# Optimization experiments

Hardware: AMD Instinct MI355X
Metric: run time of the kernel (lower is better)

## Reference

```python
import jax, jax.numpy as jnp
import numpy as np

RES = (20, 20)
SIGMA = 0.1


def setup_inputs() -> dict:
    key = jax.random.key(0)
    # [batch, num_dims, max_points, 2] birth/death coords in [0,1)
    pd = jax.random.uniform(key, (32, 3, 2048, 2), dtype=jnp.float32)
    return {"persistence_diagrams": pd}


def reference(persistence_diagrams) -> jnp.ndarray:
    # births/deaths: [B, D, P]
    births = persistence_diagrams[..., 0]
    deaths = persistence_diagrams[..., 1]
    pers = deaths - births  # persistence; also the default weight function
    # Original loop skips all-zero rows and points with persistence <= 0.
    # An all-zero row has persistence == 0, so (pers > 0) subsumes both checks.
    eff_w = jnp.where(pers > 0, pers, 0.0)  # [B, D, P]

    x_range = jnp.linspace(0.0, 1.0, RES[0], dtype=jnp.float32)
    y_range = jnp.linspace(0.0, 1.0, RES[1], dtype=jnp.float32)
    xx, yy = jnp.meshgrid(x_range, y_range, indexing="ij")  # [Rx, Ry]

    # Splat each point's Gaussian centered at (birth, persistence) onto the grid.
    # d2: [B, D, P, Rx, Ry]
    d2 = (xx - births[..., None, None]) ** 2 + (yy - pers[..., None, None]) ** 2
    gauss = jnp.exp(-d2 / (2.0 * SIGMA ** 2))
    # Weighted sum over points -> [B, D, Rx, Ry]
    image = jnp.einsum("bdpxy,bdp->bdxy", gauss, eff_w)
    return image
```

## Files before the change

### kernel.cpp

```cpp
#include <hip/hip_runtime.h>


#define RX 20
#define RY 20
#define SPLIT 8
#define CHUNK 256
#define STRIDE 22

__global__ __launch_bounds__(256) void pimg_kernel(const float2* __restrict__ pd,
                                                   float* __restrict__ out,
                                                   int n_bd) {
    __shared__ __attribute__((aligned(16))) float s_gxw[CHUNK * STRIDE];
    __shared__ __attribute__((aligned(16))) float s_gy[CHUNK * STRIDE];
    __shared__ int s_wave_cnt[4];

    const int tid   = threadIdx.x;
    const int bd    = blockIdx.x / SPLIT;
    const int chunk = blockIdx.x % SPLIT;
    const int pbase = bd * 2048 + chunk * CHUNK;

    float2 p2  = pd[pbase + tid];
    float birth = p2.x;
    float pers  = p2.y - p2.x;
    bool active = pers > 0.0f;

    unsigned long long mask = __ballot(active);
    int lane = tid & 63;
    int wid  = tid >> 6;
    int rank = __popcll(mask & ((1ull << lane) - 1ull));
    if (lane == 0) s_wave_cnt[wid] = __popcll(mask);
    __syncthreads();

    int offset = 0;
    #pragma unroll
    for (int w = 0; w < 4; ++w)
        if (w < wid) offset += s_wave_cnt[w];
    int total = s_wave_cnt[0] + s_wave_cnt[1] + s_wave_cnt[2] + s_wave_cnt[3];

    if (active) {
        int slot = offset + rank;
        #pragma unroll
        for (int i = 0; i < RX; ++i) {
            float xi = i * (1.0f / 19.0f);
            float dx = xi - birth;
            float dy = xi - pers;
            s_gxw[slot * STRIDE + i] = pers * __expf(-50.0f * dx * dx);
            s_gy [slot * STRIDE + i] =        __expf(-50.0f * dy * dy);
        }
    }
    __syncthreads();

    if (tid < 200) {
        int i  = tid / 10;
        int j0 = (tid % 10) * 2;
        float acc0 = 0.0f, acc1 = 0.0f;
        #pragma unroll 4
        for (int p = 0; p < total; ++p) {
            float  gx = s_gxw[p * STRIDE + i];
            float2 gy = *(const float2*)&s_gy[p * STRIDE + j0];
            acc0 = fmaf(gx, gy.x, acc0);
            acc1 = fmaf(gx, gy.y, acc1);
        }
        float* o = out + (bd * RX + i) * RY + j0;
        atomicAdd(o,     acc0);
        atomicAdd(o + 1, acc1);
    }
}

extern "C" void kernel_launch(void* const* d_in, const int* in_sizes, int n_in,
                              void* d_out, int out_size, void* d_ws, size_t ws_size,
                              hipStream_t stream) {
    const float2* pd = (const float2*)d_in[0];
    float* out = (float*)d_out;
    int n_bd = in_sizes[0] / (2048 * 2);
    hipMemsetAsync(d_out, 0, (size_t)out_size * sizeof(float), stream);
    pimg_kernel<<<dim3(n_bd * SPLIT), dim3(256), 0, stream>>>(pd, out, n_bd);
}
```

Baseline: 60.44 us.

## Transpose shared tables and use 2x2 register tiles with split-K reduction

Stores the per-point Gaussian factors transposed (grid index major, point index minor) so each thread can read float4 runs of points. Each thread now computes a 2x2 output tile, and two thread halves split the point range and then combine their partial sums through shared memory before the atomics. This aims to cut LDS load instructions per FMA and to use all 256 threads instead of 200. The cost is zero-padding writes to reach a multiple of four points, an extra barrier, and a strided transposed write pattern that may cause bank conflicts.

```diff
diff --git a/kernel.cpp b/kernel.cpp
--- a/kernel.cpp
+++ b/kernel.cpp
@@ -5,14 +5,15 @@
 #define RY 20
 #define SPLIT 8
 #define CHUNK 256
-#define STRIDE 22
+#define PST 260
 
 __global__ __launch_bounds__(256) void pimg_kernel(const float2* __restrict__ pd,
                                                    float* __restrict__ out,
                                                    int n_bd) {
-    __shared__ __attribute__((aligned(16))) float s_gxw[CHUNK * STRIDE];
-    __shared__ __attribute__((aligned(16))) float s_gy[CHUNK * STRIDE];
+    __shared__ __attribute__((aligned(16))) float s_gxT[RX * PST];
+    __shared__ __attribute__((aligned(16))) float s_gyT[RY * PST];
     __shared__ int s_wave_cnt[4];
+    __shared__ float s_red[100 * 5];
 
     const int tid   = threadIdx.x;
     const int bd    = blockIdx.x / SPLIT;
@@ -36,6 +37,7 @@
     for (int w = 0; w < 4; ++w)
         if (w < wid) offset += s_wave_cnt[w];
     int total = s_wave_cnt[0] + s_wave_cnt[1] + s_wave_cnt[2] + s_wave_cnt[3];
+    int tp = (total + 3) & ~3;
 
     if (active) {
         int slot = offset + rank;
@@ -44,26 +46,65 @@
             float xi = i * (1.0f / 19.0f);
             float dx = xi - birth;
             float dy = xi - pers;
-            s_gxw[slot * STRIDE + i] = pers * __expf(-50.0f * dx * dx);
-            s_gy [slot * STRIDE + i] =        __expf(-50.0f * dy * dy);
+            s_gxT[i * PST + slot] = pers * __expf(-50.0f * dx * dx);
+            s_gyT[i * PST + slot] =        __expf(-50.0f * dy * dy);
+        }
+    }
+    if (tid >= total && tid < tp) {
+        #pragma unroll
+        for (int i = 0; i < RX; ++i) {
+            s_gxT[i * PST + tid] = 0.0f;
+            s_gyT[i * PST + tid] = 0.0f;
         }
     }
     __syncthreads();
 
-    if (tid < 200) {
-        int i  = tid / 10;
-        int j0 = (tid % 10) * 2;
-        float acc0 = 0.0f, acc1 = 0.0f;
-        #pragma unroll 4
-        for (int p = 0; p < total; ++p) {
-            float  gx = s_gxw[p * STRIDE + i];
-            float2 gy = *(const float2*)&s_gy[p * STRIDE + j0];
-            acc0 = fmaf(gx, gy.x, acc0);
-            acc1 = fmaf(gx, gy.y, acc1);
+    const int half = tid >> 7;
+    const int t100 = tid & 127;
+    float a00 = 0.0f, a01 = 0.0f, a10 = 0.0f, a11 = 0.0f;
+    int ig = 0, jg = 0;
+    if (t100 < 100) {
+        ig = t100 / 10;
+        jg = t100 % 10;
+        int s_mid = (tp >> 1) & ~3;
+        int s0 = half ? s_mid : 0;
+        int s1 = half ? tp    : s_mid;
+        const float* gxa = &s_gxT[ ig       * PST];
+        const float* gxb = &s_gxT[(ig + 10) * PST];
+        const float* gya = &s_gyT[ jg       * PST];
+        const float* gyb = &s_gyT[(jg + 10) * PST];
+        for (int s = s0; s < s1; s += 4) {
+            float4 xa = *(const float4*)(gxa + s);
+            float4 xb = *(const float4*)(gxb + s);
+            float4 ya = *(const float4*)(gya + s);
+            float4 yb = *(const float4*)(gyb + s);
+            a00 = fmaf(xa.x, ya.x, a00); a00 = fmaf(xa.y, ya.y, a00);
+            a00 = fmaf(xa.z, ya.z, a00); a00 = fmaf(xa.w, ya.w, a00);
+            a01 = fmaf(xa.x, yb.x, a01); a01 = fmaf(xa.y, yb.y, a01);
+            a01 = fmaf(xa.z, yb.z, a01); a01 = fmaf(xa.w, yb.w, a01);
+            a10 = fmaf(xb.x, ya.x, a10); a10 = fmaf(xb.y, ya.y, a10);
+            a10 = fmaf(xb.z, ya.z, a10); a10 = fmaf(xb.w, ya.w, a10);
+            a11 = fmaf(xb.x, yb.x, a11); a11 = fmaf(xb.y, yb.y, a11);
+            a11 = fmaf(xb.z, yb.z, a11); a11 = fmaf(xb.w, yb.w, a11);
         }
-        float* o = out + (bd * RX + i) * RY + j0;
-        atomicAdd(o,     acc0);
-        atomicAdd(o + 1, acc1);
+    }
+    if (half == 1 && t100 < 100) {
+        s_red[t100 * 5 + 0] = a00;
+        s_red[t100 * 5 + 1] = a01;
+        s_red[t100 * 5 + 2] = a10;
+        s_red[t100 * 5 + 3] = a11;
+    }
+    __syncthreads();
+    if (half == 0 && t100 < 100) {
+        a00 += s_red[t100 * 5 + 0];
+        a01 += s_red[t100 * 5 + 1];
+        a10 += s_red[t100 * 5 + 2];
+        a11 += s_red[t100 * 5 + 3];
+        float* o = out + bd * (RX * RY);
+        atomicAdd(o +  ig       * RY + jg,      a00);
+        atomicAdd(o +  ig       * RY + jg + 10, a01);
+        atomicAdd(o + (ig + 10) * RY + jg,      a10);
+        atomicAdd(o + (ig + 10) * RY + jg + 10, a11);
     }
 }
 
```

After: 59.00 us (median of 2 runs). 1.02x faster.

## Transpose Gaussian tables, use register-tiled outer product with wave-split reduction

Applied to the files above, without the earlier changes.

Stores the x and y Gaussian factors transposed (grid index major, point minor) so the accumulation loop can read float4 vectors along points. Each lane computes a 2x4 register tile of outputs, and the point range is split across the four waves, with a shared-memory reduction before the atomics. The exponentials are now produced by a recurrence that multiplies by precomputed ratios, so only four expf calls are made per half-row instead of twenty. The recurrence can drift numerically, and the extra reduction pass adds a barrier and more shared memory.

```diff
diff --git a/kernel.cpp b/kernel.cpp
--- a/kernel.cpp
+++ b/kernel.cpp
@@ -5,65 +5,123 @@
 #define RY 20
 #define SPLIT 8
 #define CHUNK 256
-#define STRIDE 22
+#define PST 260
+#define H (1.0f / 19.0f)
+
+#define FMA4(acc, xv, yv)                                        \
+    acc = fmaf(xv.x, yv.x, acc); acc = fmaf(xv.y, yv.y, acc);    \
+    acc = fmaf(xv.z, yv.z, acc); acc = fmaf(xv.w, yv.w, acc);
 
 __global__ __launch_bounds__(256) void pimg_kernel(const float2* __restrict__ pd,
                                                    float* __restrict__ out,
                                                    int n_bd) {
-    __shared__ __attribute__((aligned(16))) float s_gxw[CHUNK * STRIDE];
-    __shared__ __attribute__((aligned(16))) float s_gy[CHUNK * STRIDE];
-    __shared__ int s_wave_cnt[4];
+    __shared__ __attribute__((aligned(16))) float s_gxT[RX * PST];
+    __shared__ __attribute__((aligned(16))) float s_gyT[RY * PST];
+    __shared__ float2 s_pts[CHUNK];
+    __shared__ float  s_red[3 * 50 * 9];
+    __shared__ int    s_wave_cnt[4];
 
-    const int tid   = threadIdx.x;
+    const int tid  = threadIdx.x;
+    const int lane = tid & 63;
+    const int wid  = tid >> 6;
     const int bd    = blockIdx.x / SPLIT;
     const int chunk = blockIdx.x % SPLIT;
     const int pbase = bd * 2048 + chunk * CHUNK;
 
-    float2 p2  = pd[pbase + tid];
+    float2 p2   = pd[pbase + tid];
     float birth = p2.x;
     float pers  = p2.y - p2.x;
     bool active = pers > 0.0f;
 
     unsigned long long mask = __ballot(active);
-    int lane = tid & 63;
-    int wid  = tid >> 6;
-    int rank = __popcll(mask & ((1ull << lane) - 1ull));
     if (lane == 0) s_wave_cnt[wid] = __popcll(mask);
     __syncthreads();
 
-    int offset = 0;
+    int offset = 0, total = 0;
     #pragma unroll
-    for (int w = 0; w < 4; ++w)
-        if (w < wid) offset += s_wave_cnt[w];
-    int total = s_wave_cnt[0] + s_wave_cnt[1] + s_wave_cnt[2] + s_wave_cnt[3];
+    for (int w = 0; w < 4; ++w) {
+        int c = s_wave_cnt[w];
+        if (w < wid) offset += c;
+        total += c;
+    }
+    int tp = (total + 3) & ~3;
+    if (active) {
+        int rank = __popcll(mask & ((1ull << lane) - 1ull));
+        s_pts[offset + rank] = make_float2(birth, pers);
+    }
+    if (tid >= total && tid < tp)
+        s_pts[tid] = make_float2(0.0f, 0.0f);
+    __syncthreads();
 
-    if (active) {
-        int slot = offset + rank;
-        #pragma unroll
-        for (int i = 0; i < RX; ++i) {
-            float xi = i * (1.0f / 19.0f);
-            float dx = xi - birth;
-            float dy = xi - pers;
-            s_gxw[slot * STRIDE + i] = pers * __expf(-50.0f * dx * dx);
-            s_gy [slot * STRIDE + i] =        __expf(-50.0f * dy * dy);
+    {
+        const int ibase = (tid & 1) * 10;
+        const float rc = __expf(-100.0f * H * H);
+        for (int s = tid >> 1; s < tp; s += 128) {
+            float2 bp = s_pts[s];
+            float b = bp.x, q = bp.y;
+            float dx = ibase * H - b;
+            float dy = ibase * H - q;
+            float fx = __expf(-50.0f * dx * dx);
+            float fy = __expf(-50.0f * dy * dy);
+            float gx = __expf(-100.0f * H * dx - 50.0f * H * H);
+            float gy = __expf(-100.0f * H * dy - 50.0f * H * H);
+            #pragma unroll
+            for (int ii = 0; ii < 10; ++ii) {
+                s_gxT[(ibase + ii) * PST + s] = q * fx;
+                s_gyT[(ibase + ii) * PST + s] = fy;
+                fx *= gx; gx *= rc;
+                fy *= gy; gy *= rc;
+            }
         }
     }
     __syncthreads();
 
-    if (tid < 200) {
-        int i  = tid / 10;
-        int j0 = (tid % 10) * 2;
-        float acc0 = 0.0f, acc1 = 0.0f;
-        #pragma unroll 4
-        for (int p = 0; p < total; ++p) {
-            float  gx = s_gxw[p * STRIDE + i];
-            float2 gy = *(const float2*)&s_gy[p * STRIDE + j0];
-            acc0 = fmaf(gx, gy.x, acc0);
-            acc1 = fmaf(gx, gy.y, acc1);
+    float a[2][4] = {{0.0f, 0.0f, 0.0f, 0.0f}, {0.0f, 0.0f, 0.0f, 0.0f}};
+    const int i0 = lane / 5;
+    const int j0 = lane % 5;
+    if (lane < 50) {
+        int qs = (((tp + 3) >> 2) + 3) & ~3;
+        int s0 = wid * qs; if (s0 > tp) s0 = tp;
+        int s1 = s0 + qs;  if (s1 > tp) s1 = tp;
+        const float* gxa = &s_gxT[ i0        * PST];
+        const float* gxb = &s_gxT[(i0 + 10)  * PST];
+        const float* gy0 = &s_gyT[ j0        * PST];
+        const float* gy1 = &s_gyT[(j0 + 5)   * PST];
+        const float* gy2 = &s_gyT[(j0 + 10)  * PST];
+        const float* gy3 = &s_gyT[(j0 + 15)  * PST];
+        for (int s = s0; s < s1; s += 4) {
+            float4 xa = *(const float4*)(gxa + s);
+            float4 xb = *(const float4*)(gxb + s);
+            float4 y0 = *(const float4*)(gy0 + s);
+            float4 y1 = *(const float4*)(gy1 + s);
+            float4 y2 = *(const float4*)(gy2 + s);
+            float4 y3 = *(const float4*)(gy3 + s);
+            FMA4(a[0][0], xa, y0); FMA4(a[0][1], xa, y1);
+            FMA4(a[0][2], xa, y2); FMA4(a[0][3], xa, y3);
+            FMA4(a[1][0], xb, y0); FMA4(a[1][1], xb, y1);
+            FMA4(a[1][2], xb, y2); FMA4(a[1][3], xb, y3);
         }
-        float* o = out + (bd * RX + i) * RY + j0;
-        atomicAdd(o,     acc0);
-        atomicAdd(o + 1, acc1);
+    }
+
+    if (wid > 0 && lane < 50) {
+        float* r = &s_red[(wid - 1) * 450 + lane * 9];
+        #pragma unroll
+        for (int k = 0; k < 8; ++k) r[k] = a[k >> 2][k & 3];
+    }
+    __syncthreads();
+    if (wid == 0 && lane < 50) {
+        #pragma unroll
+        for (int w = 0; w < 3; ++w) {
+            const float* r = &s_red[w * 450 + lane * 9];
+            #pragma unroll
+            for (int k = 0; k < 8; ++k) a[k >> 2][k & 3] += r[k];
+        }
+        float* o = out + bd * (RX * RY);
+        #pragma unroll
+        for (int rr = 0; rr < 2; ++rr)
+            #pragma unroll
+            for (int cc = 0; cc < 4; ++cc)
+                atomicAdd(o + (i0 + 10 * rr) * RY + (j0 + 5 * cc), a[rr][cc]);
     }
 }
 
```

Result: no change. 60.50 us (+0.1%).
